# Performance work log

Measured on AMD Instinct MI355X. Metric: run time of the kernel, lower is better.

Reference implementation:

```python
import jax, jax.numpy as jnp
import numpy as np

N_QUBITS = 14
N_LAYERS = 3
SCALE = 1.0
BATCH = 256


def _ry(t):
    # t: scalar () or batched (b,) float32 -> (...,2,2) complex64
    c, s = jnp.cos(t / 2), jnp.sin(t / 2)
    m = jnp.stack([jnp.stack([c, -s], axis=-1),
                   jnp.stack([s, c], axis=-1)], axis=-2)
    return m.astype(jnp.complex64)


def _rz(t):
    tc = t.astype(jnp.complex64)
    e_m = jnp.exp(-0.5j * tc)
    e_p = jnp.exp(0.5j * tc)
    z = jnp.zeros_like(e_m)
    return jnp.stack([jnp.stack([e_m, z], axis=-1),
                      jnp.stack([z, e_p], axis=-1)], axis=-2)


def _rx(t):
    c = jnp.cos(t / 2).astype(jnp.complex64)
    s = (-1j) * jnp.sin(t / 2).astype(jnp.complex64)
    return jnp.stack([jnp.stack([c, s], axis=-1),
                      jnp.stack([s, c], axis=-1)], axis=-2)


def _apply_1q(state, gate, w, n):
    # state: (b, 2**n) complex; gate: (2,2) shared or (b,2,2) per-batch
    b = state.shape[0]
    A, C = 2 ** w, 2 ** (n - w - 1)
    s = state.reshape(b, A, 2, C)
    if gate.ndim == 2:
        s = jnp.einsum('st,batc->basc', gate, s)
    else:
        s = jnp.einsum('bst,batc->basc', gate, s)
    return s.reshape(b, -1)


def _cnot(state, c, t, n):
    # flip target bit on the control=1 half of the state
    b = state.shape[0]
    lo, hi = min(c, t), max(c, t)
    A, B, C = 2 ** lo, 2 ** (hi - lo - 1), 2 ** (n - hi - 1)
    s = state.reshape(b, A, 2, B, 2, C)
    if c == lo:  # control at axis 2, target at axis 4
        s = s.at[:, :, 1].set(jnp.flip(s[:, :, 1], axis=3))
    else:        # control at axis 4, target at axis 2
        s = s.at[:, :, :, :, 1].set(jnp.flip(s[:, :, :, :, 1], axis=2))
    return s.reshape(b, -1)


def _circuit(z_batch, theta, n, scale):
    b = z_batch.shape[0]
    state = jnp.zeros((b, 2 ** n), jnp.complex64).at[:, 0].set(1.0)
    # latent encoding: per-sample RY, RZ on each wire
    for w in range(n):
        state = _apply_1q(state, _ry(z_batch[:, w]), w, n)
        state = _apply_1q(state, _rz(z_batch[:, w]), w, n)
    # variational layers
    for l in range(theta.shape[0]):
        for w in range(n):
            state = _apply_1q(state, _rx(theta[l, w, 0]), w, n)
            state = _apply_1q(state, _ry(theta[l, w, 1]), w, n)
            state = _apply_1q(state, _rz(theta[l, w, 2]), w, n)
        if n > 1:
            for w in range(n - 1):
                state = _cnot(state, w, w + 1, n)
            state = _cnot(state, n - 1, 0, n)
    # <Z_w> = P(bit_w = 0) - P(bit_w = 1)
    probs = state.real ** 2 + state.imag ** 2  # (b, 2**n)
    p = probs.reshape((b,) + (2,) * n)
    evs = []
    for w in range(n):
        axes = tuple(i + 1 for i in range(n) if i != w)
        pw = p.sum(axis=axes)  # (b, 2)
        evs.append(pw[:, 0] - pw[:, 1])
    return (scale * jnp.stack(evs, axis=1)).astype(jnp.float32)


def setup_inputs() -> dict:
    key = jax.random.key(0)
    kz, kt = jax.random.split(key)
    z_batch = jax.random.normal(kz, (BATCH, N_QUBITS), dtype=jnp.float32)
    theta = 0.02 * jax.random.normal(kt, (N_LAYERS, N_QUBITS, 3), dtype=jnp.float32)
    return {"z_batch": z_batch, "theta": theta}


def reference(z_batch, theta):
    return _circuit(z_batch, theta, N_QUBITS, SCALE)
```

## Files before the change

### kernel.cpp

```cpp
#include <hip/hip_runtime.h>


#define NQ 14
#define NS (1 << NQ)
#define NT 512
#define NLAYERS 3

typedef float c2 __attribute__((ext_vector_type(2)));

struct Sched {
    unsigned m2[NQ], r2[NQ];
    unsigned m3[NQ], r3[NQ];
    unsigned frow[NQ];
};

constexpr Sched make_sched() {
    Sched s{};
    unsigned c[NQ] = {}, r[NQ] = {};
    for (int w = 0; w < NQ; ++w) { c[w] = 1u << (NQ - 1 - w); r[w] = 1u << (NQ - 1 - w); }
    for (int ring = 0; ring < 3; ++ring) {
        for (int w = 0; w < NQ - 1; ++w) { c[w] ^= c[w + 1]; r[w + 1] ^= r[w]; }
        c[NQ - 1] ^= c[0]; r[0] ^= r[NQ - 1];
        if (ring == 0) for (int w = 0; w < NQ; ++w) { s.m2[w] = c[w]; s.r2[w] = r[w]; }
        if (ring == 1) for (int w = 0; w < NQ; ++w) { s.m3[w] = c[w]; s.r3[w] = r[w]; }
        if (ring == 2) for (int w = 0; w < NQ; ++w) { s.frow[w] = r[w]; }
    }
    return s;
}
constexpr Sched S = make_sched();

struct Meta {
    unsigned mask[4];
    unsigned row[4];
    unsigned lut[16];
    unsigned npiv;
    int K;
    int g0;
};

constexpr Meta mkpass(const unsigned* m, const unsigned* r, int w0, int K, int g0base) {
    Meta p{};
    p.K = K; p.g0 = g0base + w0;
    for (int i = 0; i < K; ++i) { p.mask[i] = m[w0 + i]; p.row[i] = r[w0 + i]; }
    unsigned red[4] = {}, pivbit[4] = {}, pivs = 0;
    for (int i = 0; i < K; ++i) {
        unsigned v = p.mask[i];
        for (int j = 0; j < i; ++j) if (v & pivbit[j]) v ^= red[j];
        unsigned hb = 0;
        for (int b = 13; b >= 0; --b) if ((v >> b) & 1u) { hb = 1u << b; break; }
        red[i] = v; pivbit[i] = hb; pivs |= hb;
    }
    p.npiv = (~pivs) & 0x3FFFu;
    for (int j = 0; j < (1 << K); ++j) {
        unsigned x = 0;
        for (int i = 0; i < K; ++i) if ((j >> i) & 1) x ^= p.mask[i];
        p.lut[j] = x;
    }
    return p;
}

constexpr Meta PM[8] = {
    mkpass(S.m2, S.r2, 0, 4, 0),  mkpass(S.m2, S.r2, 4, 4, 0),
    mkpass(S.m2, S.r2, 8, 3, 0),  mkpass(S.m2, S.r2, 11, 3, 0),
    mkpass(S.m3, S.r3, 0, 4, 14), mkpass(S.m3, S.r3, 4, 4, 14),
    mkpass(S.m3, S.r3, 8, 3, 14), mkpass(S.m3, S.r3, 11, 3, 14),
};
static_assert(__builtin_popcount(PM[0].npiv) == 10, "GE failed p0");
static_assert(__builtin_popcount(PM[2].npiv) == 11, "GE failed p2");
static_assert(__builtin_popcount(PM[5].npiv) == 10, "GE failed p5");
static_assert(__builtin_popcount(PM[7].npiv) == 11, "GE failed p7");

struct c32 { float x, y; };
__device__ __forceinline__ c32 cmul(c32 a, c32 b) {
    return c32{ a.x * b.x - a.y * b.y, a.x * b.y + a.y * b.x };
}
__device__ __forceinline__ c32 cadd(c32 a, c32 b) { return c32{ a.x + b.x, a.y + b.y }; }
__device__ __forceinline__ c2 cmulv(c2 a, c2 b) {
    return (c2){ a.x * b.x - a.y * b.y, a.x * b.y + a.y * b.x };
}

struct M2x2 { c32 a, b, c, d; };
__device__ __forceinline__ M2x2 mmul(M2x2 X, M2x2 Y) {
    M2x2 o;
    o.a = cadd(cmul(X.a, Y.a), cmul(X.b, Y.c));
    o.b = cadd(cmul(X.a, Y.b), cmul(X.b, Y.d));
    o.c = cadd(cmul(X.c, Y.a), cmul(X.d, Y.c));
    o.d = cadd(cmul(X.c, Y.b), cmul(X.d, Y.d));
    return o;
}
__device__ __forceinline__ M2x2 mRX(float c, float s) { return M2x2{ {c,0.f},{0.f,-s},{0.f,-s},{c,0.f} }; }
__device__ __forceinline__ M2x2 mRY(float c, float s) { return M2x2{ {c,0.f},{-s,0.f},{s,0.f},{c,0.f} }; }
__device__ __forceinline__ M2x2 mRZ(float c, float s) { return M2x2{ {c,-s},{0.f,0.f},{0.f,0.f},{c,s} }; }

template<int P>
__device__ __forceinline__ void do_pass(c2* st, const float4 (*gmv)[2][3], int tid) {
    constexpr Meta pm = PM[P];
    constexpr int K = pm.K;
    constexpr int NSLOT = 1 << K;
    constexpr int NCS = 1 << (5 - K);

    #pragma unroll 1
    for (int cs = 0; cs < NCS; ++cs) {
        unsigned idx = (unsigned)tid + (unsigned)(cs << 9);
        unsigned rep = 0;
        #pragma unroll
        for (int bb = 0; bb < 14; ++bb)
            if ((pm.npiv >> bb) & 1u)
                rep |= ((idx >> __builtin_popcount(pm.npiv & ((1u << bb) - 1))) & 1u) << bb;
        unsigned lt = 0;
        #pragma unroll
        for (int i = 0; i < K; ++i) lt ^= ((idx >> i) & 1u) ? pm.mask[i] : 0u;
        const unsigned repf = rep ^ lt;
        unsigned sel[4];
        #pragma unroll
        for (int i = 0; i < K; ++i) sel[i] = __popc(repf & pm.row[i]) & 1u;

        c2 e[NSLOT];
        #pragma unroll
        for (int j = 0; j < NSLOT; ++j) e[j] = st[repf ^ pm.lut[j]];

        #pragma unroll
        for (int w = 0; w < K; ++w) {
            const float4* mp = gmv[pm.g0 + w][sel[w]];
            const float4 RE = mp[0];
            const float4 I0 = mp[1];
            const float4 I1 = mp[2];
            #pragma unroll
            for (int t = 0; t < NSLOT / 2; ++t) {
                const int j  = ((t >> w) << (w + 1)) | (t & ((1 << w) - 1));
                const int j2 = j | (1 << w);
                const c2 x = e[j], y = e[j2];
                const c2 xs = __builtin_shufflevector(x, x, 1, 0);
                const c2 ys = __builtin_shufflevector(y, y, 1, 0);
                e[j]  = x * RE.x + xs * (c2){I0.x, I0.y} + y * RE.y + ys * (c2){I0.z, I0.w};
                e[j2] = x * RE.z + xs * (c2){I1.x, I1.y} + y * RE.w + ys * (c2){I1.z, I1.w};
            }
        }
        #pragma unroll
        for (int j = 0; j < NSLOT; ++j) st[repf ^ pm.lut[j]] = e[j];
    }
}

__global__ __launch_bounds__(NT, 2)
void qsim_kernel(const float* __restrict__ z, const float* __restrict__ th,
                 float* __restrict__ out)
{
    extern __shared__ c2 st[];
    __shared__ float4 gmv[28][2][3];
    __shared__ c2     vtab[NQ][2];
    __shared__ float  red[NT / 64][NQ];

    const int bq  = blockIdx.x;
    const int tid = threadIdx.x;

    if (tid < 28) {
        const int rd = tid / 14, w = tid % 14, l = rd + 1;
        const float* tp = th + (l * NQ + w) * 3;
        float s0, c0, s1, c1, s2, c2_;
        __sincosf(0.5f * tp[0], &s0, &c0);
        __sincosf(0.5f * tp[1], &s1, &c1);
        __sincosf(0.5f * tp[2], &s2, &c2_);
        const M2x2 G = mmul(mRZ(c2_, s2), mmul(mRY(c1, s1), mRX(c0, s0)));
        gmv[tid][0][0] = make_float4(G.a.x, G.b.x, G.c.x, G.d.x);
        gmv[tid][0][1] = make_float4(-G.a.y, G.a.y, -G.b.y, G.b.y);
        gmv[tid][0][2] = make_float4(-G.c.y, G.c.y, -G.d.y, G.d.y);
        gmv[tid][1][0] = make_float4(G.d.x, G.c.x, G.b.x, G.a.x);
        gmv[tid][1][1] = make_float4(-G.d.y, G.d.y, -G.c.y, G.c.y);
        gmv[tid][1][2] = make_float4(-G.b.y, G.b.y, -G.a.y, G.a.y);
    } else if (tid >= 32 && tid < 32 + NQ) {
        const int w = tid - 32;
        const float zt = z[bq * NQ + w];
        float sz_, cz_; __sincosf(0.5f * zt, &sz_, &cz_);
        const c32 a0{ cz_ * cz_, -cz_ * sz_ }, b0{ sz_ * cz_, sz_ * sz_ };
        const float* tp = th + (0 * NQ + w) * 3;
        float s0, c0, s1, c1, s2, c2_;
        __sincosf(0.5f * tp[0], &s0, &c0);
        __sincosf(0.5f * tp[1], &s1, &c1);
        __sincosf(0.5f * tp[2], &s2, &c2_);
        const M2x2 G = mmul(mRZ(c2_, s2), mmul(mRY(c1, s1), mRX(c0, s0)));
        const c32 v0 = cadd(cmul(G.a, a0), cmul(G.b, b0));
        const c32 v1 = cadd(cmul(G.c, a0), cmul(G.d, b0));
        vtab[w][0] = (c2){ v0.x, v0.y };
        vtab[w][1] = (c2){ v1.x, v1.y };
    }
    __syncthreads();

    {
        c2 pf = vtab[13][tid & 1];
        #pragma unroll
        for (int p = 1; p < 9; ++p) pf = cmulv(pf, vtab[13 - p][(tid >> p) & 1]);
        #pragma unroll 1
        for (int cs = 0; cs < 2; ++cs) {
            c2 e16[16];
            e16[0] = cmulv(pf, vtab[0][cs]);
            #pragma unroll
            for (int bb = 0; bb < 4; ++bb) {
                const c2 v0 = vtab[4 - bb][0], v1 = vtab[4 - bb][1];
                #pragma unroll
                for (int t = 0; t < (1 << bb); ++t) {
                    const c2 base = e16[t];
                    e16[t + (1 << bb)] = cmulv(base, v1);
                    e16[t] = cmulv(base, v0);
                }
            }
            #pragma unroll
            for (int t = 0; t < 16; ++t) st[tid + ((cs * 16 + t) << 9)] = e16[t];
        }
    }
    __syncthreads();

    do_pass<0>(st, gmv, tid); __syncthreads();
    do_pass<1>(st, gmv, tid); __syncthreads();
    do_pass<2>(st, gmv, tid); __syncthreads();
    do_pass<3>(st, gmv, tid); __syncthreads();
    do_pass<4>(st, gmv, tid); __syncthreads();
    do_pass<5>(st, gmv, tid); __syncthreads();
    do_pass<6>(st, gmv, tid); __syncthreads();
    do_pass<7>(st, gmv, tid); __syncthreads();

    float W[32];
    #pragma unroll
    for (int j = 0; j < 32; ++j) {
        const c2 a = st[tid + (j << 9)];
        W[j] = a.x * a.x + a.y * a.y;
    }
    #pragma unroll
    for (int bb = 0; bb < 5; ++bb) {
        #pragma unroll
        for (int t = 0; t < 16; ++t) {
            const int j  = ((t >> bb) << (bb + 1)) | (t & ((1 << bb) - 1));
            const int j2 = j | (1 << bb);
            const float u = W[j], v = W[j2];
            W[j] = u + v; W[j2] = u - v;
        }
    }
    float ev[NQ];
    #pragma unroll
    for (int w = 0; w < NQ; ++w) {
        const float val = W[S.frow[w] >> 9];
        ev[w] = (__popc((unsigned)tid & (S.frow[w] & 0x1FFu)) & 1) ? -val : val;
    }
    const int lane = tid & 63, wv = tid >> 6;
    #pragma unroll
    for (int w = 0; w < NQ; ++w) {
        float v = ev[w];
        #pragma unroll
        for (int off = 32; off > 0; off >>= 1) v += __shfl_down(v, off, 64);
        if (lane == 0) red[wv][w] = v;
    }
    __syncthreads();
    if (tid < NQ) {
        float v = 0.f;
        #pragma unroll
        for (int i = 0; i < NT / 64; ++i) v += red[i][tid];
        out[bq * NQ + tid] = v;
    }
}

extern "C" void kernel_launch(void* const* d_in, const int* in_sizes, int n_in,
                              void* d_out, int out_size, void* d_ws, size_t ws_size,
                              hipStream_t stream)
{
    (void)n_in; (void)out_size; (void)d_ws; (void)ws_size;
    const float* z  = (const float*)d_in[0];
    const float* th = (const float*)d_in[1];
    float* out = (float*)d_out;

    const int B = in_sizes[0] / NQ;

    hipFuncSetAttribute(reinterpret_cast<const void*>(qsim_kernel),
                        hipFuncAttributeMaxDynamicSharedMemorySize, NS * 8);

    qsim_kernel<<<dim3(B), dim3(NT), NS * 8, stream>>>(z, th, out);
}
```

Measured before the change: 86.49 us.

## Double block size to 1024 threads and precompute per-pass index bases

Raises the threads per block from 512 to 1024, so each thread handles half as many amplitudes in initialization, each gate pass and the final reduction. Per-pass representative-index computation is hoisted out of the chunk loop using constexpr bit-run masks, with the second chunk derived by XOR with a precomputed bit. The aim is more parallelism per statevector and less integer index arithmetic. In exchange, launch bounds of 1024 threads with 4 blocks may squeeze registers, and the 128KB LDS state still limits how many blocks fit per CU.

```diff
diff --git a/kernel.cpp b/kernel.cpp
--- a/kernel.cpp
+++ b/kernel.cpp
@@ -3,7 +3,8 @@
 
 #define NQ 14
 #define NS (1 << NQ)
-#define NT 512
+#define NT 1024
+#define NW (NT / 64)
 #define NLAYERS 3
 
 typedef float c2 __attribute__((ext_vector_type(2)));
@@ -34,6 +35,11 @@
     unsigned row[4];
     unsigned lut[16];
     unsigned npiv;
+    unsigned run_mask[10];
+    int      run_shl[10];
+    int      nruns;
+    int      pos10;
+    unsigned selhi10;
     int K;
     int g0;
 };
@@ -56,6 +62,23 @@
         for (int i = 0; i < K; ++i) if ((j >> i) & 1) x ^= p.mask[i];
         p.lut[j] = x;
     }
+    int pos[14] = {}; int nb = 0;
+    for (int b = 0; b < 14; ++b) if ((p.npiv >> b) & 1) pos[nb++] = b;
+    p.nruns = 0;
+    int k = 0;
+    while (k < 10) {
+        const int off = pos[k] - k;
+        unsigned mm = 0;
+        while (k < 10 && pos[k] - k == off) { mm |= 1u << k; ++k; }
+        p.run_mask[p.nruns] = mm;
+        p.run_shl[p.nruns] = off;
+        ++p.nruns;
+    }
+    p.pos10 = (nb > 10) ? pos[10] : 0;
+    p.selhi10 = 0;
+    if (nb > 10)
+        for (int i = 0; i < K; ++i)
+            p.selhi10 |= ((p.row[i] >> p.pos10) & 1u) << i;
     return p;
 }
 
@@ -97,23 +120,24 @@
     constexpr Meta pm = PM[P];
     constexpr int K = pm.K;
     constexpr int NSLOT = 1 << K;
-    constexpr int NCS = 1 << (5 - K);
+    constexpr int NCS = (K == 4) ? 1 : 2;
+
+    unsigned rep = 0;
+    #pragma unroll
+    for (int rn = 0; rn < pm.nruns; ++rn)
+        rep |= ((unsigned)tid & pm.run_mask[rn]) << pm.run_shl[rn];
+    unsigned lt = 0;
+    #pragma unroll
+    for (int i = 0; i < K; ++i) lt ^= ((tid >> i) & 1u) ? pm.mask[i] : 0u;
+    const unsigned base = rep ^ lt;
+    unsigned selb = 0;
+    #pragma unroll
+    for (int i = 0; i < K; ++i) selb |= (unsigned)(__popc(base & pm.row[i]) & 1) << i;
 
     #pragma unroll 1
     for (int cs = 0; cs < NCS; ++cs) {
-        unsigned idx = (unsigned)tid + (unsigned)(cs << 9);
-        unsigned rep = 0;
-        #pragma unroll
-        for (int bb = 0; bb < 14; ++bb)
-            if ((pm.npiv >> bb) & 1u)
-                rep |= ((idx >> __builtin_popcount(pm.npiv & ((1u << bb) - 1))) & 1u) << bb;
-        unsigned lt = 0;
-        #pragma unroll
-        for (int i = 0; i < K; ++i) lt ^= ((idx >> i) & 1u) ? pm.mask[i] : 0u;
-        const unsigned repf = rep ^ lt;
-        unsigned sel[4];
-        #pragma unroll
-        for (int i = 0; i < K; ++i) sel[i] = __popc(repf & pm.row[i]) & 1u;
+        const unsigned repf = cs ? (base ^ (1u << pm.pos10)) : base;
+        const unsigned sel  = cs ? (selb ^ pm.selhi10) : selb;
 
         c2 e[NSLOT];
         #pragma unroll
@@ -121,7 +145,7 @@
 
         #pragma unroll
         for (int w = 0; w < K; ++w) {
-            const float4* mp = gmv[pm.g0 + w][sel[w]];
+            const float4* mp = gmv[pm.g0 + w][(sel >> w) & 1u];
             const float4 RE = mp[0];
             const float4 I0 = mp[1];
             const float4 I1 = mp[2];
@@ -141,14 +165,14 @@
     }
 }
 
-__global__ __launch_bounds__(NT, 2)
+__global__ __launch_bounds__(NT, 4)
 void qsim_kernel(const float* __restrict__ z, const float* __restrict__ th,
                  float* __restrict__ out)
 {
     extern __shared__ c2 st[];
     __shared__ float4 gmv[28][2][3];
     __shared__ c2     vtab[NQ][2];
-    __shared__ float  red[NT / 64][NQ];
+    __shared__ float  red[NW][NQ];
 
     const int bq  = blockIdx.x;
     const int tid = threadIdx.x;
@@ -188,24 +212,21 @@
     {
         c2 pf = vtab[13][tid & 1];
         #pragma unroll
-        for (int p = 1; p < 9; ++p) pf = cmulv(pf, vtab[13 - p][(tid >> p) & 1]);
-        #pragma unroll 1
-        for (int cs = 0; cs < 2; ++cs) {
-            c2 e16[16];
-            e16[0] = cmulv(pf, vtab[0][cs]);
+        for (int p = 1; p < 10; ++p) pf = cmulv(pf, vtab[13 - p][(tid >> p) & 1]);
+        c2 e16[16];
+        e16[0] = pf;
+        #pragma unroll
+        for (int bb = 0; bb < 4; ++bb) {
+            const c2 v0 = vtab[3 - bb][0], v1 = vtab[3 - bb][1];
             #pragma unroll
-            for (int bb = 0; bb < 4; ++bb) {
-                const c2 v0 = vtab[4 - bb][0], v1 = vtab[4 - bb][1];
-                #pragma unroll
-                for (int t = 0; t < (1 << bb); ++t) {
-                    const c2 base = e16[t];
-                    e16[t + (1 << bb)] = cmulv(base, v1);
-                    e16[t] = cmulv(base, v0);
-                }
+            for (int t = 0; t < (1 << bb); ++t) {
+                const c2 base = e16[t];
+                e16[t + (1 << bb)] = cmulv(base, v1);
+                e16[t] = cmulv(base, v0);
             }
-            #pragma unroll
-            for (int t = 0; t < 16; ++t) st[tid + ((cs * 16 + t) << 9)] = e16[t];
         }
+        #pragma unroll
+        for (int j = 0; j < 16; ++j) st[tid + (j << 10)] = e16[j];
     }
     __syncthreads();
 
@@ -218,16 +239,16 @@
     do_pass<6>(st, gmv, tid); __syncthreads();
     do_pass<7>(st, gmv, tid); __syncthreads();
 
-    float W[32];
-    #pragma unroll
-    for (int j = 0; j < 32; ++j) {
-        const c2 a = st[tid + (j << 9)];
+    float W[16];
+    #pragma unroll
+    for (int j = 0; j < 16; ++j) {
+        const c2 a = st[tid + (j << 10)];
         W[j] = a.x * a.x + a.y * a.y;
     }
     #pragma unroll
-    for (int bb = 0; bb < 5; ++bb) {
-        #pragma unroll
-        for (int t = 0; t < 16; ++t) {
+    for (int bb = 0; bb < 4; ++bb) {
+        #pragma unroll
+        for (int t = 0; t < 8; ++t) {
             const int j  = ((t >> bb) << (bb + 1)) | (t & ((1 << bb) - 1));
             const int j2 = j | (1 << bb);
             const float u = W[j], v = W[j2];
@@ -237,8 +258,8 @@
     float ev[NQ];
     #pragma unroll
     for (int w = 0; w < NQ; ++w) {
-        const float val = W[S.frow[w] >> 9];
-        ev[w] = (__popc((unsigned)tid & (S.frow[w] & 0x1FFu)) & 1) ? -val : val;
+        const float val = W[S.frow[w] >> 10];
+        ev[w] = (__popc((unsigned)tid & (S.frow[w] & 0x3FFu)) & 1) ? -val : val;
     }
     const int lane = tid & 63, wv = tid >> 6;
     #pragma unroll
@@ -252,7 +273,7 @@
     if (tid < NQ) {
         float v = 0.f;
         #pragma unroll
-        for (int i = 0; i < NT / 64; ++i) v += red[i][tid];
+        for (int i = 0; i < NW; ++i) v += red[i][tid];
         out[bq * NQ + tid] = v;
     }
 }
```

Measured after the change: 84.52 us. 2.3% less time.

## Fuse five qubits per shared-memory pass to cut pass count from eight to six

Applied to the files above, without the earlier changes.

Each layer's 14 fused single-qubit gates are now regrouped into passes of 5,5,4 qubits instead of 4,4,3,3. Two full read/write sweeps of the 128KB shared-memory state and two block barriers go away. Per-thread index computation is hoisted out of the chunk loop using precomputed bit-run shifts and a single high-bit toggle for the second chunk. In exchange, each thread holds 32 complex amplitudes in registers for the K=5 passes, which raises register pressure and may affect occupancy under launch_bounds(512,2).

```diff
diff --git a/kernel.cpp b/kernel.cpp
--- a/kernel.cpp
+++ b/kernel.cpp
@@ -4,6 +4,8 @@
 #define NQ 14
 #define NS (1 << NQ)
 #define NT 512
+#define NTB 9
+#define NW (NT / 64)
 #define NLAYERS 3
 
 typedef float c2 __attribute__((ext_vector_type(2)));
@@ -30,10 +32,15 @@
 constexpr Sched S = make_sched();
 
 struct Meta {
-    unsigned mask[4];
-    unsigned row[4];
-    unsigned lut[16];
+    unsigned mask[5];
+    unsigned row[5];
+    unsigned lut[32];
     unsigned npiv;
+    unsigned run_mask[NTB];
+    int      run_shl[NTB];
+    int      nruns;
+    int      posC;
+    unsigned selhiC;
     int K;
     int g0;
 };
@@ -42,7 +49,7 @@
     Meta p{};
     p.K = K; p.g0 = g0base + w0;
     for (int i = 0; i < K; ++i) { p.mask[i] = m[w0 + i]; p.row[i] = r[w0 + i]; }
-    unsigned red[4] = {}, pivbit[4] = {}, pivs = 0;
+    unsigned red[5] = {}, pivbit[5] = {}, pivs = 0;
     for (int i = 0; i < K; ++i) {
         unsigned v = p.mask[i];
         for (int j = 0; j < i; ++j) if (v & pivbit[j]) v ^= red[j];
@@ -56,19 +63,36 @@
         for (int i = 0; i < K; ++i) if ((j >> i) & 1) x ^= p.mask[i];
         p.lut[j] = x;
     }
+    int pos[14] = {}; int nb = 0;
+    for (int b = 0; b < 14; ++b) if ((p.npiv >> b) & 1) pos[nb++] = b;
+    p.nruns = 0;
+    int k = 0;
+    while (k < NTB) {
+        const int off = pos[k] - k;
+        unsigned mm = 0;
+        while (k < NTB && pos[k] - k == off) { mm |= 1u << k; ++k; }
+        p.run_mask[p.nruns] = mm;
+        p.run_shl[p.nruns] = off;
+        ++p.nruns;
+    }
+    p.posC = (nb > NTB) ? pos[NTB] : 0;
+    p.selhiC = 0;
+    if (nb > NTB)
+        for (int i = 0; i < K; ++i)
+            p.selhiC |= ((p.row[i] >> p.posC) & 1u) << i;
     return p;
 }
 
-constexpr Meta PM[8] = {
-    mkpass(S.m2, S.r2, 0, 4, 0),  mkpass(S.m2, S.r2, 4, 4, 0),
-    mkpass(S.m2, S.r2, 8, 3, 0),  mkpass(S.m2, S.r2, 11, 3, 0),
-    mkpass(S.m3, S.r3, 0, 4, 14), mkpass(S.m3, S.r3, 4, 4, 14),
-    mkpass(S.m3, S.r3, 8, 3, 14), mkpass(S.m3, S.r3, 11, 3, 14),
+constexpr Meta PM[6] = {
+    mkpass(S.m2, S.r2, 0, 5, 0),  mkpass(S.m2, S.r2, 5, 5, 0),  mkpass(S.m2, S.r2, 10, 4, 0),
+    mkpass(S.m3, S.r3, 0, 5, 14), mkpass(S.m3, S.r3, 5, 5, 14), mkpass(S.m3, S.r3, 10, 4, 14),
 };
-static_assert(__builtin_popcount(PM[0].npiv) == 10, "GE failed p0");
-static_assert(__builtin_popcount(PM[2].npiv) == 11, "GE failed p2");
+static_assert(__builtin_popcount(PM[0].npiv) == 9,  "GE failed p0");
+static_assert(__builtin_popcount(PM[1].npiv) == 9,  "GE failed p1");
+static_assert(__builtin_popcount(PM[2].npiv) == 10, "GE failed p2");
+static_assert(__builtin_popcount(PM[3].npiv) == 9,  "GE failed p3");
+static_assert(__builtin_popcount(PM[4].npiv) == 9,  "GE failed p4");
 static_assert(__builtin_popcount(PM[5].npiv) == 10, "GE failed p5");
-static_assert(__builtin_popcount(PM[7].npiv) == 11, "GE failed p7");
 
 struct c32 { float x, y; };
 __device__ __forceinline__ c32 cmul(c32 a, c32 b) {
@@ -97,23 +121,24 @@
     constexpr Meta pm = PM[P];
     constexpr int K = pm.K;
     constexpr int NSLOT = 1 << K;
-    constexpr int NCS = 1 << (5 - K);
+    constexpr int NCS = (K == 5) ? 1 : 2;
+
+    unsigned rep = 0;
+    #pragma unroll
+    for (int rn = 0; rn < pm.nruns; ++rn)
+        rep |= ((unsigned)tid & pm.run_mask[rn]) << pm.run_shl[rn];
+    unsigned lt = 0;
+    #pragma unroll
+    for (int i = 0; i < K; ++i) lt ^= ((tid >> i) & 1u) ? pm.mask[i] : 0u;
+    const unsigned base = rep ^ lt;
+    unsigned selb = 0;
+    #pragma unroll
+    for (int i = 0; i < K; ++i) selb |= (unsigned)(__popc(base & pm.row[i]) & 1) << i;
 
     #pragma unroll 1
     for (int cs = 0; cs < NCS; ++cs) {
-        unsigned idx = (unsigned)tid + (unsigned)(cs << 9);
-        unsigned rep = 0;
-        #pragma unroll
-        for (int bb = 0; bb < 14; ++bb)
-            if ((pm.npiv >> bb) & 1u)
-                rep |= ((idx >> __builtin_popcount(pm.npiv & ((1u << bb) - 1))) & 1u) << bb;
-        unsigned lt = 0;
-        #pragma unroll
-        for (int i = 0; i < K; ++i) lt ^= ((idx >> i) & 1u) ? pm.mask[i] : 0u;
-        const unsigned repf = rep ^ lt;
-        unsigned sel[4];
-        #pragma unroll
-        for (int i = 0; i < K; ++i) sel[i] = __popc(repf & pm.row[i]) & 1u;
+        const unsigned repf = cs ? (base ^ (1u << pm.posC)) : base;
+        const unsigned sel  = cs ? (selb ^ pm.selhiC) : selb;
 
         c2 e[NSLOT];
         #pragma unroll
@@ -121,7 +146,7 @@
 
         #pragma unroll
         for (int w = 0; w < K; ++w) {
-            const float4* mp = gmv[pm.g0 + w][sel[w]];
+            const float4* mp = gmv[pm.g0 + w][(sel >> w) & 1u];
             const float4 RE = mp[0];
             const float4 I0 = mp[1];
             const float4 I1 = mp[2];
@@ -148,7 +173,7 @@
     extern __shared__ c2 st[];
     __shared__ float4 gmv[28][2][3];
     __shared__ c2     vtab[NQ][2];
-    __shared__ float  red[NT / 64][NQ];
+    __shared__ float  red[NW][NQ];
 
     const int bq  = blockIdx.x;
     const int tid = threadIdx.x;
@@ -215,8 +240,6 @@
     do_pass<3>(st, gmv, tid); __syncthreads();
     do_pass<4>(st, gmv, tid); __syncthreads();
     do_pass<5>(st, gmv, tid); __syncthreads();
-    do_pass<6>(st, gmv, tid); __syncthreads();
-    do_pass<7>(st, gmv, tid); __syncthreads();
 
     float W[32];
     #pragma unroll
@@ -252,7 +275,7 @@
     if (tid < NQ) {
         float v = 0.f;
         #pragma unroll
-        for (int i = 0; i < NT / 64; ++i) v += red[i][tid];
+        for (int i = 0; i < NW; ++i) v += red[i][tid];
         out[bq * NQ + tid] = v;
     }
 }
```

After: 82.48 us. -4.6%, faster.
